# Kernel optimization log

Hardware: AMD Instinct MI355X
Metric: run time of the kernel (lower is better)

The kernel has to match this reference:

```python
import jax, jax.numpy as jnp
import numpy as np

N_TARGET = 1_000_000
GRID = 220
C_IN, C_OUT = 32, 64
BN_EPS = 1e-5


def _build_topology():
    # Real sparse-voxel topology: random occupied cells in a GRID^3 volume.
    rng = np.random.default_rng(0)
    raw = rng.integers(0, GRID, size=(1_400_000, 3), dtype=np.int64)
    keys = np.unique((raw[:, 0] * GRID + raw[:, 1]) * GRID + raw[:, 2])[:N_TARGET]
    N = keys.shape[0]
    coords = np.stack([keys // (GRID * GRID), (keys // GRID) % GRID, keys % GRID], axis=1)
    # Rulebook: for each of the 27 kernel offsets, index of the neighbor voxel (N = missing -> zero pad row).
    nbr = np.full((N, 27), N, dtype=np.int32)
    k = 0
    for dx in (-1, 0, 1):
        for dy in (-1, 0, 1):
            for dz in (-1, 0, 1):
                nc = coords + np.array([dx, dy, dz])
                valid = np.all((nc >= 0) & (nc < GRID), axis=1)
                nk = (nc[:, 0] * GRID + nc[:, 1]) * GRID + nc[:, 2]
                pos = np.clip(np.searchsorted(keys, nk), 0, N - 1)
                found = valid & (keys[pos] == nk)
                nbr[found, k] = pos[found].astype(np.int32)
                k += 1
    # MaxPool(2,2): voxels sharing coords//2 pool together.
    PG = GRID // 2 + 1
    pkeys = ((coords[:, 0] // 2) * PG + coords[:, 1] // 2) * PG + coords[:, 2] // 2
    uniq, pool_ids = np.unique(pkeys, return_inverse=True)
    return N, nbr, pool_ids.astype(np.int32), int(uniq.shape[0])


def setup_inputs() -> dict:
    N, nbr, pool_ids, num_pooled = _build_topology()
    key = jax.random.key(0)
    k1, k2, k3 = jax.random.split(key, 3)
    return {
        "feats": jax.random.normal(k1, (N, C_IN), dtype=jnp.float32),
        "W1": jax.random.normal(k2, (27, C_IN, C_OUT), dtype=jnp.float32) * 0.1,
        "gamma1": jnp.ones((C_OUT,), jnp.float32),
        "beta1": jnp.zeros((C_OUT,), jnp.float32),
        "W2": jax.random.normal(k3, (27, C_OUT, C_OUT), dtype=jnp.float32) * 0.1,
        "gamma2": jnp.ones((C_OUT,), jnp.float32),
        "beta2": jnp.zeros((C_OUT,), jnp.float32),
        "nbr_idx": jnp.asarray(nbr),
        "pool_ids": jnp.asarray(pool_ids),
        "num_pooled": num_pooled,
    }


def _sparse_conv3(f, W, nbr_idx):
    # f: [N, Cin], W: [27, Cin, Cout], nbr_idx: [N, 27] with pad index N.
    N = f.shape[0]
    fp = jnp.concatenate([f, jnp.zeros((1, f.shape[1]), f.dtype)], axis=0)  # zero pad row
    out = jnp.zeros((N, W.shape[2]), f.dtype)
    for k in range(27):  # fixed kernel offsets: gather -> GEMM -> accumulate
        out = out + fp[nbr_idx[:, k]] @ W[k]
    return out


def _batch_norm(f, gamma, beta):
    # Training-mode BN over the voxel dim (biased variance), as torch BatchNorm.
    m = f.mean(axis=0)
    v = f.var(axis=0)
    return (f - m) * jax.lax.rsqrt(v + BN_EPS) * gamma + beta


def reference(feats, W1, gamma1, beta1, W2, gamma2, beta2, nbr_idx, pool_ids, num_pooled):
    x = jax.nn.relu(_batch_norm(_sparse_conv3(feats, W1, nbr_idx), gamma1, beta1))
    x = _batch_norm(_sparse_conv3(x, W2, nbr_idx), gamma2, beta2)
    pooled = jax.ops.segment_max(x, pool_ids, num_segments=num_pooled)
    return x, pooled
```

## Files before the change

### kernel.cpp

```cpp
#include <hip/hip_runtime.h>
#include <hip/hip_bf16.h>
#include <stdint.h>

#define TPB 256

typedef __bf16 bf16x8 __attribute__((ext_vector_type(8)));
typedef float f32x4 __attribute__((ext_vector_type(4)));
union U16x8 { uint4 u; bf16x8 b; };

typedef const uint32_t __attribute__((address_space(1))) glb_u32;
typedef uint32_t __attribute__((address_space(3))) lds_u32;

template <int N> __device__ __forceinline__ void stage_wait_barrier() {
  asm volatile("s_waitcnt vmcnt(%0)" :: "i"(N) : "memory");
  __builtin_amdgcn_s_barrier();
  __builtin_amdgcn_sched_barrier(0);
}

__device__ __forceinline__ float bfbits2f(uint32_t lo16) {
  union { uint32_t u; float f; } c; c.u = lo16 << 16; return c.f;
}
__device__ __forceinline__ uint16_t f2bf_rne(float f) {
  union { float f; uint32_t u; } c; c.f = f;
  uint32_t r = 0x7FFFu + ((c.u >> 16) & 1u);
  return (uint16_t)((c.u + r) >> 16);
}

__global__ __launch_bounds__(TPB) void prep_w_kernel(
    const float* __restrict__ W1, const float* __restrict__ W2,
    uint16_t* __restrict__ w1t, uint16_t* __restrict__ w2t)
{
  int i = blockIdx.x * TPB + threadIdx.x;
  if (i < 27 * 2048) {
    int k = i >> 11, cin = (i >> 6) & 31, cout = i & 63;
    int cin2 = (((cin >> 3) ^ (cout & 3)) << 3) | (cin & 7);
    w1t[(k << 11) + (cout << 5) + cin2] = f2bf_rne(W1[i]);
  } else {
    int j = i - 27 * 2048;
    if (j < 27 * 4096) {
      int k = j >> 12, cin = (j >> 6) & 63, cout = j & 63;
      int cin2 = (((cin >> 3) ^ (cout & 7)) << 3) | (cin & 7);
      w2t[(k << 12) + (cout << 6) + cin2] = f2bf_rne(W2[j]);
    }
  }
}

__global__ __launch_bounds__(TPB) void prep_x0_kernel(
    const float* __restrict__ feats, uint16_t* __restrict__ x0, long long N)
{
  long long t = (long long)blockIdx.x * TPB + threadIdx.x;
  if (t >= (N + 1) * 4) return;
  long long e = t * 8;
  uint4 o;
  if (e < N * 32) {
    float4 a = *(const float4*)(feats + e);
    float4 b = *(const float4*)(feats + e + 4);
    o.x = (uint32_t)f2bf_rne(a.x) | ((uint32_t)f2bf_rne(a.y) << 16);
    o.y = (uint32_t)f2bf_rne(a.z) | ((uint32_t)f2bf_rne(a.w) << 16);
    o.z = (uint32_t)f2bf_rne(b.x) | ((uint32_t)f2bf_rne(b.y) << 16);
    o.w = (uint32_t)f2bf_rne(b.z) | ((uint32_t)f2bf_rne(b.w) << 16);
  } else {
    o.x = o.y = o.z = o.w = 0;
  }
  *(uint4*)(x0 + e) = o;
}

__global__ __launch_bounds__(TPB) void bucket_build_kernel(
    const int* __restrict__ pool_ids, int* __restrict__ count,
    int* __restrict__ members, long long N)
{
  long long i = (long long)blockIdx.x * TPB + threadIdx.x;
  if (i < N) {
    int pid = pool_ids[i];
    int slot = atomicAdd(&count[pid], 1);
    members[(long long)pid * 8 + slot] = (int)i;
  }
}

template <int CIN, int R, int OCC>
__global__ __launch_bounds__(TPB, OCC) void conv_mfma_kernel(
    const uint16_t* __restrict__ x, const uint16_t* __restrict__ wt,
    const int* __restrict__ nbr, uint16_t* __restrict__ yb,
    float* __restrict__ statsrep, int N)
{
  constexpr int CHUNKS = CIN / 32;
  constexpr int LOGROWB = (CIN == 32) ? 6 : 7;
  constexpr int SWZ = (CIN == 32) ? 3 : 7;
  constexpr int WKB = 64 * CIN * 2;
  constexpr int NW = WKB / (TPB * 16);
  constexpr int NG = R * CHUNKS;
  constexpr int ROWS = 4 * R * 16;
  constexpr int NINTS = ROWS * 27;
  constexpr int NCH16 = NINTS / 4;

  __shared__ __align__(16) char Wlds[2][WKB];
  __shared__ __align__(16) int nbrLds[NINTS];
  __shared__ float sred[4][128];

  const int tid = threadIdx.x;
  const int lane = tid & 63;
  const int wave = tid >> 6;
  const int l15 = lane & 15;
  const int l4 = lane >> 4;

  int bid;
  {
    int nwg = gridDim.x, q = nwg >> 3, r = nwg & 7;
    int xcd = blockIdx.x & 7, pos = blockIdx.x >> 3;
    bid = (xcd < r ? xcd * (q + 1) : r * (q + 1) + (xcd - r) * q) + pos;
  }
  const long long row0 = (long long)bid * ROWS;

  f32x4 acc[R][4];
#pragma unroll
  for (int r = 0; r < R; ++r)
#pragma unroll
    for (int t = 0; t < 4; ++t)
      acc[r][t] = (f32x4){0.f, 0.f, 0.f, 0.f};

  {
    const char* nsrc = (const char*)nbr + row0 * 108;
    long long blkB = (long long)N * 108 - row0 * 108;
    int fullChunks = (int)(blkB >> 4);
    if (fullChunks > NCH16) fullChunks = NCH16;
#pragma unroll
    for (int u = 0; u < (NCH16 + TPB - 1) / TPB; ++u) {
      int idx = u * TPB + tid;
      if (idx < fullChunks)
        __builtin_amdgcn_global_load_lds((glb_u32*)(nsrc + idx * 16),
                                         (lds_u32*)((char*)nbrLds + idx * 16), 16, 0, 0);
    }
    for (int ii = fullChunks * 4 + tid; ii < NINTS; ii += TPB) {
      long long gi = row0 * 27 + ii;
      nbrLds[ii] = (gi < (long long)N * 27) ? nbr[gi] : N;
    }
  }

  auto stageW = [&](int k, int b) {
    const char* src = (const char*)(wt + (size_t)k * 64 * CIN);
#pragma unroll
    for (int u = 0; u < NW; ++u) {
      int off = (tid + u * TPB) * 16;
      __builtin_amdgcn_global_load_lds((glb_u32*)(src + off),
                                       (lds_u32*)(&Wlds[b][off]), 16, 0, 0);
    }
  };
  auto gather = [&](int k, U16x8 (&dst)[R][CHUNKS]) {
#pragma unroll
    for (int r = 0; r < R; ++r) {
      int lrow = (wave * R + r) * 16 + l15;
      int g = nbrLds[lrow * 27 + k];
      const uint16_t* xr = x + (size_t)g * CIN + (l4 << 3);
#pragma unroll
      for (int c = 0; c < CHUNKS; ++c)
        dst[r][c].u = *(const uint4*)(xr + c * 32);
    }
  };
  auto compute = [&](int wsel, U16x8 (&xs)[R][CHUNKS]) {
    bf16x8 bfrag[4][CHUNKS];
#pragma unroll
    for (int t = 0; t < 4; ++t) {
      int n = t * 16 + l15;
#pragma unroll
      for (int c = 0; c < CHUNKS; ++c) {
        int colb = (l4 << 4) + (c << 6);
        int d = (n << LOGROWB) | (colb ^ ((n & SWZ) << 4));
        U16x8 tmp; tmp.u = *(const uint4*)(&Wlds[wsel][d]);
        bfrag[t][c] = tmp.b;
      }
    }
#pragma unroll
    for (int r = 0; r < R; ++r)
#pragma unroll
      for (int c = 0; c < CHUNKS; ++c)
#pragma unroll
        for (int t = 0; t < 4; ++t)
          acc[r][t] = __builtin_amdgcn_mfma_f32_16x16x32_bf16(
              xs[r][c].b, bfrag[t][c], acc[r][t], 0, 0, 0);
  };

  U16x8 xA[R][CHUNKS], xB[R][CHUNKS];

  stageW(0, 0);
  __syncthreads();
  gather(0, xA);

#pragma unroll 1
  for (int kk = 0; kk < 13; ++kk) {
    stageW(2 * kk + 1, 1);
    __builtin_amdgcn_sched_barrier(0);
    gather(2 * kk + 1, xB);
    compute(0, xA);
    stage_wait_barrier<NG>();
    stageW(2 * kk + 2, 0);
    __builtin_amdgcn_sched_barrier(0);
    gather(2 * kk + 2, xA);
    compute(1, xB);
    stage_wait_barrier<NG>();
  }
  compute(0, xA);

#pragma unroll
  for (int r = 0; r < R; ++r) {
    long long vr0 = row0 + (wave * R + r) * 16 + (l4 << 2);
#pragma unroll
    for (int reg = 0; reg < 4; ++reg) {
      long long vr = vr0 + reg;
      if (vr < N) {
        uint16_t* yr = yb + vr * 64 + l15;
#pragma unroll
        for (int t = 0; t < 4; ++t) yr[t * 16] = f2bf_rne(acc[r][t][reg]);
      }
    }
  }

  float s[4], s2[4];
#pragma unroll
  for (int t = 0; t < 4; ++t) { s[t] = 0.f; s2[t] = 0.f; }
#pragma unroll
  for (int r = 0; r < R; ++r) {
    long long vr0 = row0 + (wave * R + r) * 16 + (l4 << 2);
#pragma unroll
    for (int reg = 0; reg < 4; ++reg) {
      if (vr0 + reg < N) {
#pragma unroll
        for (int t = 0; t < 4; ++t) {
          float v = acc[r][t][reg];
          s[t] += v;
          s2[t] = fmaf(v, v, s2[t]);
        }
      }
    }
  }
#pragma unroll
  for (int t = 0; t < 4; ++t) {
    s[t] += __shfl_xor(s[t], 16);
    s[t] += __shfl_xor(s[t], 32);
    s2[t] += __shfl_xor(s2[t], 16);
    s2[t] += __shfl_xor(s2[t], 32);
  }
  __syncthreads();
  if (l4 == 0) {
#pragma unroll
    for (int t = 0; t < 4; ++t) {
      sred[wave][t * 16 + l15] = s[t];
      sred[wave][64 + t * 16 + l15] = s2[t];
    }
  }
  __syncthreads();
  if (tid < 128) {
    float tot = sred[0][tid] + sred[1][tid] + sred[2][tid] + sred[3][tid];
    atomicAdd(&statsrep[(bid & 15) * 128 + tid], tot);
  }
}

__global__ void bn_finalize_kernel(const float* __restrict__ reps,
                                   float* __restrict__ fin, float n)
{
  int c = threadIdx.x;
  float s = 0.f, s2 = 0.f;
  for (int r = 0; r < 16; ++r) { s += reps[r * 128 + c]; s2 += reps[r * 128 + 64 + c]; }
  float mean = s / n;
  float var = s2 / n - mean * mean;
  fin[c] = mean;
  fin[64 + c] = rsqrtf(var + 1e-5f);
}

__global__ __launch_bounds__(TPB) void bn_relu_bf16_kernel(
    const uint16_t* __restrict__ yb, const float* __restrict__ fin,
    const float* __restrict__ gamma, const float* __restrict__ beta,
    uint16_t* __restrict__ x1, long long N)
{
  long long e = ((long long)blockIdx.x * TPB + threadIdx.x) * 8;
  if (e >= (N + 1) * 64) return;
  long long row = e >> 6;
  int c = (int)(e & 63);
  uint4 out;
  if (row < N) {
    uint4 v = *(const uint4*)(yb + e);
    const uint32_t vv[4] = {v.x, v.y, v.z, v.w};
    uint32_t res[4];
#pragma unroll
    for (int q = 0; q < 4; ++q) {
      int cc = c + q * 2;
      float a0 = bfbits2f(vv[q] & 0xFFFFu);
      float a1 = bfbits2f(vv[q] >> 16);
      float o0 = fmaf((a0 - fin[cc]) * fin[64 + cc], gamma[cc], beta[cc]);
      float o1 = fmaf((a1 - fin[cc + 1]) * fin[64 + cc + 1], gamma[cc + 1], beta[cc + 1]);
      o0 = o0 > 0.f ? o0 : 0.f;
      o1 = o1 > 0.f ? o1 : 0.f;
      res[q] = (uint32_t)f2bf_rne(o0) | ((uint32_t)f2bf_rne(o1) << 16);
    }
    out.x = res[0]; out.y = res[1]; out.z = res[2]; out.w = res[3];
  } else {
    out.x = out.y = out.z = out.w = 0;
  }
  *(uint4*)(x1 + e) = out;
}

__global__ __launch_bounds__(TPB) void pool_max_write_kernel(
    const uint16_t* __restrict__ yb, const float* __restrict__ fin,
    const float* __restrict__ gamma, const float* __restrict__ beta,
    const int* __restrict__ count, const int* __restrict__ members,
    float* __restrict__ xout, float* __restrict__ pooled, long long P)
{
  long long pid = (long long)blockIdx.x * 16 + (threadIdx.x >> 4);
  if (pid >= P) return;
  int c0 = (threadIdx.x & 15) * 4;
  float4 m = *(const float4*)(fin + c0);
  float4 r = *(const float4*)(fin + 64 + c0);
  float4 g = *(const float4*)(gamma + c0);
  float4 b = *(const float4*)(beta + c0);
  int cnt = count[pid];
  float4 acc = {-3.4e38f, -3.4e38f, -3.4e38f, -3.4e38f};
  const int* mem = members + pid * 8;
  for (int t = 0; t < cnt; ++t) {
    long long row = mem[t];
    ushort4 v = *(const ushort4*)(yb + row * 64 + c0);
    float4 o;
    o.x = fmaf((bfbits2f(v.x) - m.x) * r.x, g.x, b.x);
    o.y = fmaf((bfbits2f(v.y) - m.y) * r.y, g.y, b.y);
    o.z = fmaf((bfbits2f(v.z) - m.z) * r.z, g.z, b.z);
    o.w = fmaf((bfbits2f(v.w) - m.w) * r.w, g.w, b.w);
    *(float4*)(xout + row * 64 + c0) = o;
    acc.x = fmaxf(acc.x, o.x);
    acc.y = fmaxf(acc.y, o.y);
    acc.z = fmaxf(acc.z, o.z);
    acc.w = fmaxf(acc.w, o.w);
  }
  *(float4*)(pooled + pid * 64 + c0) = acc;
}

extern "C" void kernel_launch(void* const* d_in, const int* in_sizes, int n_in,
                              void* d_out, int out_size, void* d_ws, size_t ws_size,
                              hipStream_t stream)
{
  const float* feats  = (const float*)d_in[0];
  const float* W1     = (const float*)d_in[1];
  const float* gamma1 = (const float*)d_in[2];
  const float* beta1  = (const float*)d_in[3];
  const float* W2     = (const float*)d_in[4];
  const float* gamma2 = (const float*)d_in[5];
  const float* beta2  = (const float*)d_in[6];
  const int* nbr      = (const int*)d_in[7];
  const int* pool_ids = (const int*)d_in[8];

  const long long N = (long long)in_sizes[0] / 32;
  const long long P = (long long)out_size / 64 - N;

  char* ws = (char*)d_ws;
  uint16_t* yb = (uint16_t*)ws;
  size_t y_bytes = ((size_t)N * 64 * 2 + 255) & ~(size_t)255;
  char* regB = ws + y_bytes;
  size_t regB_bytes = ((size_t)(N + 1) * 64 * 2 + 255) & ~(size_t)255;
  uint16_t* x0 = (uint16_t*)regB;
  uint16_t* x1 = (uint16_t*)regB;
  float* reps1 = (float*)(regB + regB_bytes);
  float* reps2 = reps1 + 16 * 128;
  float* fin1 = reps2 + 16 * 128;
  float* fin2 = fin1 + 128;
  int* count   = (int*)(fin2 + 128);
  int* members = count + P;

  float* xout = (float*)d_out;
  float* pooled = xout + (size_t)N * 64;
  uint16_t* w1t = (uint16_t*)pooled;
  uint16_t* w2t = w1t + 27 * 2048;

  hipMemsetAsync(reps1, 0, 2 * 16 * 128 * sizeof(float), stream);
  hipMemsetAsync(count, 0, (size_t)P * 4, stream);

  prep_w_kernel<<<(27 * 2048 + 27 * 4096 + TPB - 1) / TPB, TPB, 0, stream>>>(W1, W2, w1t, w2t);
  prep_x0_kernel<<<(int)(((N + 1) * 4 + TPB - 1) / TPB), TPB, 0, stream>>>(feats, x0, N);
  bucket_build_kernel<<<(int)((N + TPB - 1) / TPB), TPB, 0, stream>>>(pool_ids, count, members, N);

  const int convBlocks = (int)((N + 127) / 128);
  conv_mfma_kernel<32, 2, 4><<<convBlocks, TPB, 0, stream>>>(x0, w1t, nbr, yb, reps1, (int)N);
  bn_finalize_kernel<<<1, 64, 0, stream>>>(reps1, fin1, (float)N);

  long long t1 = ((N + 1) * 64) / 8;
  bn_relu_bf16_kernel<<<(int)((t1 + TPB - 1) / TPB), TPB, 0, stream>>>(
      yb, fin1, gamma1, beta1, x1, N);

  conv_mfma_kernel<64, 2, 3><<<convBlocks, TPB, 0, stream>>>(x1, w2t, nbr, yb, reps2, (int)N);
  bn_finalize_kernel<<<1, 64, 0, stream>>>(reps2, fin2, (float)N);

  pool_max_write_kernel<<<(int)((P + 15) / 16), TPB, 0, stream>>>(
      yb, fin2, gamma2, beta2, count, members, xout, pooled, P);
}
```

Measured before the change: 693.3 us.

## Load conv weights directly into registers instead of staging through LDS

Drops the double-buffered LDS staging of per-offset weight tiles and the per-stage barrier. Each wave now loads its MFMA B fragments straight from global/L2 into registers, using a new unswizzled, chunk-major weight layout. Neighbor indices are prefetched two offsets ahead so the gathers can be issued earlier. This removes the block-wide syncs and the LDS traffic, but each wave now fetches the full weights redundantly from cache and register pressure rises.

```diff
diff --git a/kernel.cpp b/kernel.cpp
--- a/kernel.cpp
+++ b/kernel.cpp
@@ -10,12 +10,6 @@
 
 typedef const uint32_t __attribute__((address_space(1))) glb_u32;
 typedef uint32_t __attribute__((address_space(3))) lds_u32;
-
-template <int N> __device__ __forceinline__ void stage_wait_barrier() {
-  asm volatile("s_waitcnt vmcnt(%0)" :: "i"(N) : "memory");
-  __builtin_amdgcn_s_barrier();
-  __builtin_amdgcn_sched_barrier(0);
-}
 
 __device__ __forceinline__ float bfbits2f(uint32_t lo16) {
   union { uint32_t u; float f; } c; c.u = lo16 << 16; return c.f;
@@ -33,14 +27,12 @@
   int i = blockIdx.x * TPB + threadIdx.x;
   if (i < 27 * 2048) {
     int k = i >> 11, cin = (i >> 6) & 31, cout = i & 63;
-    int cin2 = (((cin >> 3) ^ (cout & 3)) << 3) | (cin & 7);
-    w1t[(k << 11) + (cout << 5) + cin2] = f2bf_rne(W1[i]);
+    w1t[(k * 64 + cout) * 32 + cin] = f2bf_rne(W1[i]);
   } else {
     int j = i - 27 * 2048;
     if (j < 27 * 4096) {
       int k = j >> 12, cin = (j >> 6) & 63, cout = j & 63;
-      int cin2 = (((cin >> 3) ^ (cout & 7)) << 3) | (cin & 7);
-      w2t[(k << 12) + (cout << 6) + cin2] = f2bf_rne(W2[j]);
+      w2t[(((size_t)k * 2 + (cin >> 5)) * 64 + cout) * 32 + (cin & 31)] = f2bf_rne(W2[j]);
     }
   }
 }
@@ -84,16 +76,10 @@
     float* __restrict__ statsrep, int N)
 {
   constexpr int CHUNKS = CIN / 32;
-  constexpr int LOGROWB = (CIN == 32) ? 6 : 7;
-  constexpr int SWZ = (CIN == 32) ? 3 : 7;
-  constexpr int WKB = 64 * CIN * 2;
-  constexpr int NW = WKB / (TPB * 16);
-  constexpr int NG = R * CHUNKS;
   constexpr int ROWS = 4 * R * 16;
   constexpr int NINTS = ROWS * 27;
   constexpr int NCH16 = NINTS / 4;
 
-  __shared__ __align__(16) char Wlds[2][WKB];
   __shared__ __align__(16) int nbrLds[NINTS];
   __shared__ float sred[4][128];
 
@@ -136,39 +122,29 @@
     }
   }
 
-  auto stageW = [&](int k, int b) {
-    const char* src = (const char*)(wt + (size_t)k * 64 * CIN);
-#pragma unroll
-    for (int u = 0; u < NW; ++u) {
-      int off = (tid + u * TPB) * 16;
-      __builtin_amdgcn_global_load_lds((glb_u32*)(src + off),
-                                       (lds_u32*)(&Wlds[b][off]), 16, 0, 0);
-    }
+  auto readG = [&](int k, int (&g)[R]) {
+#pragma unroll
+    for (int r = 0; r < R; ++r)
+      g[r] = nbrLds[((wave * R + r) * 16 + l15) * 27 + k];
   };
-  auto gather = [&](int k, U16x8 (&dst)[R][CHUNKS]) {
+  auto gatherG = [&](const int (&g)[R], U16x8 (&dst)[R][CHUNKS]) {
 #pragma unroll
     for (int r = 0; r < R; ++r) {
-      int lrow = (wave * R + r) * 16 + l15;
-      int g = nbrLds[lrow * 27 + k];
-      const uint16_t* xr = x + (size_t)g * CIN + (l4 << 3);
+      const uint16_t* xr = x + (size_t)g[r] * CIN + (l4 << 3);
 #pragma unroll
       for (int c = 0; c < CHUNKS; ++c)
         dst[r][c].u = *(const uint4*)(xr + c * 32);
     }
   };
-  auto compute = [&](int wsel, U16x8 (&xs)[R][CHUNKS]) {
-    bf16x8 bfrag[4][CHUNKS];
-#pragma unroll
-    for (int t = 0; t < 4; ++t) {
-      int n = t * 16 + l15;
-#pragma unroll
-      for (int c = 0; c < CHUNKS; ++c) {
-        int colb = (l4 << 4) + (c << 6);
-        int d = (n << LOGROWB) | (colb ^ ((n & SWZ) << 4));
-        U16x8 tmp; tmp.u = *(const uint4*)(&Wlds[wsel][d]);
-        bfrag[t][c] = tmp.b;
-      }
-    }
+  auto loadW = [&](int k, U16x8 (&w)[4][CHUNKS]) {
+#pragma unroll
+    for (int t = 0; t < 4; ++t)
+#pragma unroll
+      for (int c = 0; c < CHUNKS; ++c)
+        w[t][c].u = *(const uint4*)(wt +
+            (((size_t)k * CHUNKS + c) * 64 + t * 16 + l15) * 32 + (l4 << 3));
+  };
+  auto compute = [&](U16x8 (&w)[4][CHUNKS], U16x8 (&xs)[R][CHUNKS]) {
 #pragma unroll
     for (int r = 0; r < R; ++r)
 #pragma unroll
@@ -176,29 +152,36 @@
 #pragma unroll
         for (int t = 0; t < 4; ++t)
           acc[r][t] = __builtin_amdgcn_mfma_f32_16x16x32_bf16(
-              xs[r][c].b, bfrag[t][c], acc[r][t], 0, 0, 0);
+              xs[r][c].b, w[t][c].b, acc[r][t], 0, 0, 0);
   };
 
   U16x8 xA[R][CHUNKS], xB[R][CHUNKS];
-
-  stageW(0, 0);
+  U16x8 wA[4][CHUNKS], wB[4][CHUNKS];
+  int gA2[R], gB2[R], g0[R], g1[R];
+
   __syncthreads();
-  gather(0, xA);
+  readG(0, g0); readG(1, g1);
+  gatherG(g0, xA); loadW(0, wA);
+  gatherG(g1, xB); loadW(1, wB);
+  readG(2, gA2); readG(3, gB2);
+  __builtin_amdgcn_sched_barrier(0);
 
 #pragma unroll 1
   for (int kk = 0; kk < 13; ++kk) {
-    stageW(2 * kk + 1, 1);
+    compute(wA, xA);
+    gatherG(gA2, xA);
+    loadW(2 * kk + 2, wA);
+    if (kk < 12) readG(2 * kk + 4, gA2);
     __builtin_amdgcn_sched_barrier(0);
-    gather(2 * kk + 1, xB);
-    compute(0, xA);
-    stage_wait_barrier<NG>();
-    stageW(2 * kk + 2, 0);
-    __builtin_amdgcn_sched_barrier(0);
-    gather(2 * kk + 2, xA);
-    compute(1, xB);
-    stage_wait_barrier<NG>();
-  }
-  compute(0, xA);
+    compute(wB, xB);
+    if (kk < 12) {
+      gatherG(gB2, xB);
+      loadW(2 * kk + 3, wB);
+      if (kk < 11) readG(2 * kk + 5, gB2);
+      __builtin_amdgcn_sched_barrier(0);
+    }
+  }
+  compute(wA, xA);
 
 #pragma unroll
   for (int r = 0; r < R; ++r) {
```

New measurement: 1.085 ms. 1.56x slower.
